# Optimization experiments

Measured on AMD Instinct MI355X. Metric: run time of the kernel, lower is better.

## Reference

```python
import jax, jax.numpy as jnp
import numpy as np

HS = 128  # hidden_size
B, L = 2, 1024


def setup_inputs() -> dict:
    key = jax.random.key(0)
    k = jax.random.split(key, 3)
    d = HS
    X = jax.random.normal(k[0], (B, L, d), dtype=jnp.float32)
    # mlp: Linear(4d -> d), GELU, Linear(d -> 1)
    W1 = jax.random.normal(k[1], (4 * d, d), dtype=jnp.float32) / np.sqrt(4 * d).astype(np.float32)
    b1 = jnp.zeros((d,), dtype=jnp.float32)
    W2 = jax.random.normal(k[2], (d, 1), dtype=jnp.float32) / np.sqrt(d).astype(np.float32)
    b2 = jnp.zeros((1,), dtype=jnp.float32)
    return {"X": X, "W1": W1, "b1": b1, "W2": W2, "b2": b2}


def reference(X, W1, b1, W2, b2):
    # f = cat([Xi, Xj, Xi-Xj, Xi*Xj]) @ W1  decomposes exactly into four matmuls:
    #   Xi@(Wi+Wd) + Xj@(Wj-Wd) + (Xi*Xj)@Wp
    # avoiding the (b,l,l,4d) concat tensor.
    b, l, d = X.shape
    Wi, Wj, Wd, Wp = jnp.split(W1, 4, axis=0)  # each (d, h)
    A = X @ (Wi + Wd)                           # (b,l,h): depends on i only
    Bm = X @ (Wj - Wd)                          # (b,l,h): depends on j only
    P = jnp.einsum('bid,bjd,dh->bijh', X, X, Wp)  # elementwise-product term
    h = jax.nn.gelu(A[:, :, None, :] + Bm[:, None, :, :] + P + b1,
                    approximate=False)          # (b,l,l,h), exact GELU like nn.GELU()
    out = jnp.einsum('bijh,ho->bij', h, W2) + b2[0]  # (b,l,l)
    out = jax.nn.relu(out)
    out = 0.5 * (out + jnp.swapaxes(out, 1, 2))      # symmetrize
    diag_mask = 1.0 - jnp.eye(l, dtype=out.dtype)    # zero the diagonal
    return out * diag_mask
```

## Files before the change

kernel.cpp:

```cpp
#include <hip/hip_runtime.h>


typedef __attribute__((ext_vector_type(8))) short short8;
typedef __attribute__((ext_vector_type(16))) float f32x16;
typedef __attribute__((ext_vector_type(2))) float f32x2;

#define NT 32
#define NTRI 528
#define IPB 16

__device__ __forceinline__ unsigned short f2bf(float f) {
  unsigned int u = __float_as_uint(f);
  u = (u + 0x7fffu + ((u >> 16) & 1u)) >> 16;
  return (unsigned short)u;
}

__device__ __forceinline__ short8 pack8(float4 a, float4 b) {
  short8 r;
  r[0] = (short)f2bf(a.x); r[1] = (short)f2bf(a.y);
  r[2] = (short)f2bf(a.z); r[3] = (short)f2bf(a.w);
  r[4] = (short)f2bf(b.x); r[5] = (short)f2bf(b.y);
  r[6] = (short)f2bf(b.z); r[7] = (short)f2bf(b.w);
  return r;
}

__device__ __forceinline__ f32x2 gelu_2(f32x2 x) {
  f32x2 t = x * x;
  f32x2 u = x * __builtin_elementwise_fma(t, (f32x2)0.10295205f, (f32x2)2.30220725f);
  f32x2 e;
  e[0] = __builtin_amdgcn_exp2f(u[0]);
  e[1] = __builtin_amdgcn_exp2f(u[1]);
  f32x2 ep = e + 1.0f;
  f32x2 r;
  r[0] = __builtin_amdgcn_rcpf(ep[0]);
  r[1] = __builtin_amdgcn_rcpf(ep[1]);
  return __builtin_elementwise_fma(-x, r, x);
}

__global__ void k0_prep_w(const float* __restrict__ W1, unsigned short* __restrict__ wsT) {
  int idx = blockIdx.x * 256 + threadIdx.x;
  int arr = idx >> 14, rem = idx & 16383, h = rem >> 7, d = rem & 127;
  float v;
  if (arr == 0)      v = W1[d * 128 + h] + W1[(256 + d) * 128 + h];
  else if (arr == 1) v = W1[(128 + d) * 128 + h] - W1[(256 + d) * 128 + h];
  else               v = W1[(384 + d) * 128 + h];
  wsT[idx] = f2bf(v);
}

__global__ __launch_bounds__(256) void k1_ab(const float* __restrict__ X,
                                             const unsigned short* __restrict__ wsT,
                                             const float* __restrict__ b1,
                                             float* __restrict__ Aout,
                                             float* __restrict__ Bout) {
  int tid = threadIdx.x, w = tid >> 6, lane = tid & 63, jl = lane & 31, hi = lane >> 5;
  int row0 = blockIdx.x * 64;
  int c0 = w * 64;
  f32x16 a00 = (f32x16)0.f, a01 = (f32x16)0.f, a10 = (f32x16)0.f, a11 = (f32x16)0.f;
#pragma unroll
  for (int s = 0; s < 8; ++s) {
    const float* xp0 = X + (size_t)(row0 + jl) * 128 + s * 16 + hi * 8;
    const float* xp1 = xp0 + 32 * 128;
    short8 fa0 = pack8(*(const float4*)xp0, *(const float4*)(xp0 + 4));
    short8 fa1 = pack8(*(const float4*)xp1, *(const float4*)(xp1 + 4));
    short8 fb0 = *(const short8*)(wsT + (size_t)(c0 + jl) * 128 + s * 16 + hi * 8);
    short8 fb1 = *(const short8*)(wsT + (size_t)(c0 + 32 + jl) * 128 + s * 16 + hi * 8);
    a00 = __builtin_amdgcn_mfma_f32_32x32x16_bf16(fa0, fb0, a00, 0, 0, 0);
    a01 = __builtin_amdgcn_mfma_f32_32x32x16_bf16(fa0, fb1, a01, 0, 0, 0);
    a10 = __builtin_amdgcn_mfma_f32_32x32x16_bf16(fa1, fb0, a10, 0, 0, 0);
    a11 = __builtin_amdgcn_mfma_f32_32x32x16_bf16(fa1, fb1, a11, 0, 0, 0);
  }
  bool isB = (c0 >= 128);
  float b1v0 = 0.f, b1v1 = 0.f;
  if (isB) { b1v0 = b1[c0 - 128 + jl]; b1v1 = b1[c0 - 96 + jl]; }
#pragma unroll
  for (int q = 0; q < 16; ++q) {
    int r = (q & 3) + 8 * (q >> 2) + 4 * hi;
    int bl0 = row0 + r, bl1 = row0 + 32 + r;
    if (!isB) {
      Aout[(size_t)bl0 * 128 + c0 + jl]      = a00[q];
      Aout[(size_t)bl0 * 128 + c0 + 32 + jl] = a01[q];
      Aout[(size_t)bl1 * 128 + c0 + jl]      = a10[q];
      Aout[(size_t)bl1 * 128 + c0 + 32 + jl] = a11[q];
    } else {
      Bout[(size_t)bl0 * 128 + c0 - 128 + jl] = a00[q] + b1v0;
      Bout[(size_t)bl0 * 128 + c0 - 96 + jl]  = a01[q] + b1v1;
      Bout[(size_t)bl1 * 128 + c0 - 128 + jl] = a10[q] + b1v0;
      Bout[(size_t)bl1 * 128 + c0 - 96 + jl]  = a11[q] + b1v1;
    }
  }
}

union BfPack { __bf16 h[16]; short8 v[2]; };

__global__ __launch_bounds__(256) void k2_main(const float* __restrict__ X,
                                               const unsigned short* __restrict__ WpT,
                                               const float* __restrict__ Aws,
                                               const float* __restrict__ Bws,
                                               const float* __restrict__ W2,
                                               const float* __restrict__ b2,
                                               float* __restrict__ out) {
  __shared__ __align__(16) unsigned short Mlds[2][32 * 128];
  __shared__ float2 osum[2][4][32];
  __shared__ float valbuf[IPB][33];

  int bid = blockIdx.x;
  int half = bid & 1;
  int tl = bid >> 1;
  int b = tl / NTRI;
  int t = tl - b * NTRI;
  int ti = 0;
  while (t >= NT - ti) { t -= NT - ti; ++ti; }
  int tj = ti + t;
  int gi0 = ti * 32, gj0 = tj * 32;
  int giBase = gi0 + half * IPB;

  int tid = threadIdx.x, w = tid >> 6, lane = tid & 63, jl = lane & 31, hi = lane >> 5;
  int dseg = tid >> 5;
  int gj = gj0 + jl;
  const size_t rowX = (size_t)b * 1024;

  float xj[16], bmj[16], ajv[16], w2h[16];
  {
    const float* xjp = X + (rowX + gj0 + jl) * 128 + dseg * 16;
    *(float4*)(xj + 0)  = *(const float4*)(xjp + 0);
    *(float4*)(xj + 4)  = *(const float4*)(xjp + 4);
    *(float4*)(xj + 8)  = *(const float4*)(xjp + 8);
    *(float4*)(xj + 12) = *(const float4*)(xjp + 12);
  }
#pragma unroll
  for (int g = 0; g < 4; ++g) {
    int hb = 8 * g + 4 * hi + 32 * w;
    *(float4*)(bmj + 4 * g) = *(const float4*)(Bws + (rowX + gj) * 128 + hb);
    *(float4*)(ajv + 4 * g) = *(const float4*)(Aws + (rowX + gj) * 128 + hb);
    *(float4*)(w2h + 4 * g) = *(const float4*)(W2 + hb);
  }
  short8 afrag[8];
#pragma unroll
  for (int s = 0; s < 8; ++s)
    afrag[s] = *(const short8*)(WpT + (size_t)(w * 32 + jl) * 128 + s * 16 + hi * 8);
  float b2s = b2[0];

  char* mB0 = (char*)Mlds[0];
  char* mB1 = (char*)Mlds[1];
  int rbase = jl * 256;
  int swz = (jl & 15) << 4;

  auto buildM = [&](int gi, char* mp) {
    const float* xip = X + (rowX + gi) * 128 + dseg * 16;
    float xv[16];
    *(float4*)(xv + 0)  = *(const float4*)(xip + 0);
    *(float4*)(xv + 4)  = *(const float4*)(xip + 4);
    *(float4*)(xv + 8)  = *(const float4*)(xip + 8);
    *(float4*)(xv + 12) = *(const float4*)(xip + 12);
    BfPack mb;
#pragma unroll
    for (int r = 0; r < 8; ++r) {
      f32x2 xa = { xv[2 * r], xv[2 * r + 1] };
      f32x2 xb = { xj[2 * r], xj[2 * r + 1] };
      f32x2 pr = xa * xb;
      mb.h[2 * r]     = (__bf16)pr[0];
      mb.h[2 * r + 1] = (__bf16)pr[1];
    }
    *(short8*)(mp + rbase + ((dseg * 32 + 0) ^ swz))  = mb.v[0];
    *(short8*)(mp + rbase + ((dseg * 32 + 16) ^ swz)) = mb.v[1];
  };
  auto loadBias = [&](int gi, float* aiv, float* biv) {
#pragma unroll
    for (int g = 0; g < 4; ++g) {
      int hb = 8 * g + 4 * hi + 32 * w;
      *(float4*)(aiv + 4 * g) = *(const float4*)(Aws + (rowX + gi) * 128 + hb);
      *(float4*)(biv + 4 * g) = *(const float4*)(Bws + (rowX + gi) * 128 + hb);
    }
  };
  auto mfmaTile = [&](const char* mr) -> f32x16 {
    f32x16 acc = (f32x16)0.0f;
#pragma unroll
    for (int s = 0; s < 8; ++s) {
      short8 bf = *(const short8*)(mr + rbase + (((2 * s + hi) * 16) ^ swz));
      acc = __builtin_amdgcn_mfma_f32_32x32x16_bf16(afrag[s], bf, acc, 0, 0, 0);
    }
    return acc;
  };
  auto epilogue = [&](const f32x16& acc, const float* aiv, const float* biv, int slot) {
    f32x2 o1v = { 0.f, 0.f }, o2v = { 0.f, 0.f };
#pragma unroll
    for (int k = 0; k < 8; ++k) {
      f32x2 p   = { acc[2 * k], acc[2 * k + 1] };
      f32x2 a_i = { aiv[2 * k], aiv[2 * k + 1] };
      f32x2 b_i = { biv[2 * k], biv[2 * k + 1] };
      f32x2 a_j = { ajv[2 * k], ajv[2 * k + 1] };
      f32x2 b_j = { bmj[2 * k], bmj[2 * k + 1] };
      f32x2 wv  = { w2h[2 * k], w2h[2 * k + 1] };
      f32x2 g1 = gelu_2((p + a_i) + b_j);
      f32x2 g2 = gelu_2((p + a_j) + b_i);
      o1v = __builtin_elementwise_fma(g1, wv, o1v);
      o2v = __builtin_elementwise_fma(g2, wv, o2v);
    }
    float o1 = o1v[0] + o1v[1], o2 = o2v[0] + o2v[1];
    o1 += __shfl_xor(o1, 32);
    o2 += __shfl_xor(o2, 32);
    if (lane < 32) { osum[slot][w][lane] = make_float2(o1, o2); }
  };
  auto finalize = [&](int r, int slot) {
    int j = (w << 3) + lane;
    float2 p0 = osum[slot][0][j], p1 = osum[slot][1][j];
    float2 p2 = osum[slot][2][j], p3 = osum[slot][3][j];
    float s1 = p0.x + p1.x + p2.x + p3.x + b2s;
    float s2 = p0.y + p1.y + p2.y + p3.y + b2s;
    float v = 0.5f * (fmaxf(s1, 0.f) + fmaxf(s2, 0.f));
    int gi = giBase + r;
    if (ti == tj && gj0 + j == gi) v = 0.f;
    out[(rowX + gi) * 1024 + gj0 + j] = v;
    valbuf[r][j] = v;
  };

  buildM(giBase + 0, mB0);
  __syncthreads();
  f32x16 accP = mfmaTile(mB0);
  buildM(giBase + 1, mB1);
  __syncthreads();

#pragma unroll 2
  for (int i = 1; i < IPB; ++i) {
    if (i >= 2 && lane < 8) finalize(i - 2, (i - 2) & 1);
    float aivP[16], bivP[16];
    loadBias(giBase + i - 1, aivP, bivP);
    f32x16 accC = mfmaTile((i & 1) ? mB1 : mB0);
    epilogue(accP, aivP, bivP, (i - 1) & 1);
    if (i + 1 < IPB) buildM(giBase + i + 1, ((i + 1) & 1) ? mB1 : mB0);
    accP = accC;
    __syncthreads();
  }

  if (lane < 8) finalize(IPB - 2, (IPB - 2) & 1);
  {
    float aivP[16], bivP[16];
    loadBias(giBase + IPB - 1, aivP, bivP);
    epilogue(accP, aivP, bivP, (IPB - 1) & 1);
  }
  __syncthreads();
  if (lane < 8) finalize(IPB - 1, (IPB - 1) & 1);
  __syncthreads();

  if (ti != tj && tid < 128) {
    int j = tid >> 2, i0 = (tid & 3) * 4;
    float4 v;
    v.x = valbuf[i0 + 0][j]; v.y = valbuf[i0 + 1][j];
    v.z = valbuf[i0 + 2][j]; v.w = valbuf[i0 + 3][j];
    *(float4*)(out + (rowX + gj0 + j) * 1024 + giBase + i0) = v;
  }
}

extern "C" void kernel_launch(void* const* d_in, const int* in_sizes, int n_in,
                              void* d_out, int out_size, void* d_ws, size_t ws_size,
                              hipStream_t stream) {
  (void)in_sizes; (void)n_in; (void)out_size; (void)ws_size;
  const float* X  = (const float*)d_in[0];
  const float* W1 = (const float*)d_in[1];
  const float* b1 = (const float*)d_in[2];
  const float* W2 = (const float*)d_in[3];
  const float* b2 = (const float*)d_in[4];
  float* out = (float*)d_out;

  unsigned short* wsT = (unsigned short*)d_ws;
  unsigned short* WpT = wsT + 2 * 16384;
  float* Aws = (float*)((char*)d_ws + 98304);
  float* Bws = (float*)((char*)d_ws + 98304 + 1048576);

  k0_prep_w<<<192, 256, 0, stream>>>(W1, wsT);
  k1_ab<<<32, 256, 0, stream>>>(X, wsT, b1, Aws, Bws);
  k2_main<<<4 * NTRI, 256, 0, stream>>>(X, WpT, Aws, Bws, W2, b2, out);
}
```

Measured before the change: 156.7 us.

## Stage per-row bias in LDS and restructure i-loop to single-stage pipeline

Preloads the 16 rows of A/B bias and W2 into shared memory once per block, replacing per-iteration global loads and register-held W2 with LDS reads. The MFMA/epilogue loop drops its software pipelining (previous accumulator overlapped with current MFMA) and instead prefetches the next X row into registers while computing the current tile. This cuts global traffic and register pressure, but the epilogue now waits directly on the current MFMA result, so there is less overlap between MFMA and the GELU work. LDS use also grows by about 16 KB per block.

New measurement: 146.5 us. 1.07x faster.

```diff
diff --git a/kernel.cpp b/kernel.cpp
--- a/kernel.cpp
+++ b/kernel.cpp
@@ -100,6 +100,9 @@
                                                const float* __restrict__ b2,
                                                float* __restrict__ out) {
   __shared__ __align__(16) unsigned short Mlds[2][32 * 128];
+  __shared__ __align__(16) float Abias[IPB][128];
+  __shared__ __align__(16) float Bbias[IPB][128];
+  __shared__ __align__(16) float W2l[128];
   __shared__ float2 osum[2][4][32];
   __shared__ float valbuf[IPB][33];
 
@@ -119,7 +122,7 @@
   int gj = gj0 + jl;
   const size_t rowX = (size_t)b * 1024;
 
-  float xj[16], bmj[16], ajv[16], w2h[16];
+  float xj[16], bmj[16], ajv[16];
   {
     const float* xjp = X + (rowX + gj0 + jl) * 128 + dseg * 16;
     *(float4*)(xj + 0)  = *(const float4*)(xjp + 0);
@@ -132,7 +135,6 @@
     int hb = 8 * g + 4 * hi + 32 * w;
     *(float4*)(bmj + 4 * g) = *(const float4*)(Bws + (rowX + gj) * 128 + hb);
     *(float4*)(ajv + 4 * g) = *(const float4*)(Aws + (rowX + gj) * 128 + hb);
-    *(float4*)(w2h + 4 * g) = *(const float4*)(W2 + hb);
   }
   short8 afrag[8];
 #pragma unroll
@@ -145,13 +147,25 @@
   int rbase = jl * 256;
   int swz = (jl & 15) << 4;
 
-  auto buildM = [&](int gi, char* mp) {
+  {
+    int r = tid >> 4, c = (tid & 15) * 8;
+    const float* ap = Aws + (rowX + giBase + r) * 128 + c;
+    const float* bp = Bws + (rowX + giBase + r) * 128 + c;
+    *(float4*)(&Abias[r][c])     = *(const float4*)(ap);
+    *(float4*)(&Abias[r][c + 4]) = *(const float4*)(ap + 4);
+    *(float4*)(&Bbias[r][c])     = *(const float4*)(bp);
+    *(float4*)(&Bbias[r][c + 4]) = *(const float4*)(bp + 4);
+    if (tid < 128) W2l[tid] = W2[tid];
+  }
+
+  auto loadXrow = [&](int gi, float* xv) {
     const float* xip = X + (rowX + gi) * 128 + dseg * 16;
-    float xv[16];
     *(float4*)(xv + 0)  = *(const float4*)(xip + 0);
     *(float4*)(xv + 4)  = *(const float4*)(xip + 4);
     *(float4*)(xv + 8)  = *(const float4*)(xip + 8);
     *(float4*)(xv + 12) = *(const float4*)(xip + 12);
+  };
+  auto writeM = [&](const float* xv, char* mp) {
     BfPack mb;
 #pragma unroll
     for (int r = 0; r < 8; ++r) {
@@ -164,14 +178,6 @@
     *(short8*)(mp + rbase + ((dseg * 32 + 0) ^ swz))  = mb.v[0];
     *(short8*)(mp + rbase + ((dseg * 32 + 16) ^ swz)) = mb.v[1];
   };
-  auto loadBias = [&](int gi, float* aiv, float* biv) {
-#pragma unroll
-    for (int g = 0; g < 4; ++g) {
-      int hb = 8 * g + 4 * hi + 32 * w;
-      *(float4*)(aiv + 4 * g) = *(const float4*)(Aws + (rowX + gi) * 128 + hb);
-      *(float4*)(biv + 4 * g) = *(const float4*)(Bws + (rowX + gi) * 128 + hb);
-    }
-  };
   auto mfmaTile = [&](const char* mr) -> f32x16 {
     f32x16 acc = (f32x16)0.0f;
 #pragma unroll
@@ -180,26 +186,6 @@
       acc = __builtin_amdgcn_mfma_f32_32x32x16_bf16(afrag[s], bf, acc, 0, 0, 0);
     }
     return acc;
-  };
-  auto epilogue = [&](const f32x16& acc, const float* aiv, const float* biv, int slot) {
-    f32x2 o1v = { 0.f, 0.f }, o2v = { 0.f, 0.f };
-#pragma unroll
-    for (int k = 0; k < 8; ++k) {
-      f32x2 p   = { acc[2 * k], acc[2 * k + 1] };
-      f32x2 a_i = { aiv[2 * k], aiv[2 * k + 1] };
-      f32x2 b_i = { biv[2 * k], biv[2 * k + 1] };
-      f32x2 a_j = { ajv[2 * k], ajv[2 * k + 1] };
-      f32x2 b_j = { bmj[2 * k], bmj[2 * k + 1] };
-      f32x2 wv  = { w2h[2 * k], w2h[2 * k + 1] };
-      f32x2 g1 = gelu_2((p + a_i) + b_j);
-      f32x2 g2 = gelu_2((p + a_j) + b_i);
-      o1v = __builtin_elementwise_fma(g1, wv, o1v);
-      o2v = __builtin_elementwise_fma(g2, wv, o2v);
-    }
-    float o1 = o1v[0] + o1v[1], o2 = o2v[0] + o2v[1];
-    o1 += __shfl_xor(o1, 32);
-    o2 += __shfl_xor(o2, 32);
-    if (lane < 32) { osum[slot][w][lane] = make_float2(o1, o2); }
   };
   auto finalize = [&](int r, int slot) {
     int j = (w << 3) + lane;
@@ -214,31 +200,51 @@
     valbuf[r][j] = v;
   };
 
-  buildM(giBase + 0, mB0);
+  {
+    float xv0[16];
+    loadXrow(giBase + 0, xv0);
+    writeM(xv0, mB0);
+  }
   __syncthreads();
-  f32x16 accP = mfmaTile(mB0);
-  buildM(giBase + 1, mB1);
-  __syncthreads();
 
 #pragma unroll 2
-  for (int i = 1; i < IPB; ++i) {
-    if (i >= 2 && lane < 8) finalize(i - 2, (i - 2) & 1);
-    float aivP[16], bivP[16];
-    loadBias(giBase + i - 1, aivP, bivP);
-    f32x16 accC = mfmaTile((i & 1) ? mB1 : mB0);
-    epilogue(accP, aivP, bivP, (i - 1) & 1);
-    if (i + 1 < IPB) buildM(giBase + i + 1, ((i + 1) & 1) ? mB1 : mB0);
-    accP = accC;
+  for (int i = 0; i < IPB; ++i) {
+    float xvN[16];
+    if (i + 1 < IPB) loadXrow(giBase + i + 1, xvN);
+    float aiv[16], biv[16], w2h[16];
+#pragma unroll
+    for (int g = 0; g < 4; ++g) {
+      int hb = 8 * g + 4 * hi + 32 * w;
+      *(float4*)(aiv + 4 * g) = *(const float4*)(&Abias[i][hb]);
+      *(float4*)(biv + 4 * g) = *(const float4*)(&Bbias[i][hb]);
+      *(float4*)(w2h + 4 * g) = *(const float4*)(&W2l[hb]);
+    }
+    f32x16 acc = mfmaTile((i & 1) ? mB1 : mB0);
+    if (i >= 1 && lane < 8) finalize(i - 1, (i - 1) & 1);
+    {
+      f32x2 o1v = { 0.f, 0.f }, o2v = { 0.f, 0.f };
+#pragma unroll
+      for (int k = 0; k < 8; ++k) {
+        f32x2 p   = { acc[2 * k], acc[2 * k + 1] };
+        f32x2 a_i = { aiv[2 * k], aiv[2 * k + 1] };
+        f32x2 b_i = { biv[2 * k], biv[2 * k + 1] };
+        f32x2 a_j = { ajv[2 * k], ajv[2 * k + 1] };
+        f32x2 b_j = { bmj[2 * k], bmj[2 * k + 1] };
+        f32x2 wv  = { w2h[2 * k], w2h[2 * k + 1] };
+        f32x2 g1 = gelu_2((p + a_i) + b_j);
+        f32x2 g2 = gelu_2((p + a_j) + b_i);
+        o1v = __builtin_elementwise_fma(g1, wv, o1v);
+        o2v = __builtin_elementwise_fma(g2, wv, o2v);
+      }
+      float o1 = o1v[0] + o1v[1], o2 = o2v[0] + o2v[1];
+      o1 += __shfl_xor(o1, 32);
+      o2 += __shfl_xor(o2, 32);
+      if (lane < 32) { osum[i & 1][w][lane] = make_float2(o1, o2); }
+    }
+    if (i + 1 < IPB) writeM(xvN, ((i + 1) & 1) ? mB1 : mB0);
     __syncthreads();
   }
 
-  if (lane < 8) finalize(IPB - 2, (IPB - 2) & 1);
-  {
-    float aivP[16], bivP[16];
-    loadBias(giBase + IPB - 1, aivP, bivP);
-    epilogue(accP, aivP, bivP, (IPB - 1) & 1);
-  }
-  __syncthreads();
   if (lane < 8) finalize(IPB - 1, (IPB - 1) & 1);
   __syncthreads();
 
```
